# Kernel tuning notes

Measured on AMD Instinct MI355X. Metric: run time of the kernel, lower is better.

The kernel has to match this reference:

```python
import jax, jax.numpy as jnp
import numpy as np

LN_EPS = 1e-5
SLOPE = 0.01  # LeakyReLU default

def _ln(x, g, b):
    m = x.mean(-1, keepdims=True)
    v = ((x - m) ** 2).mean(-1, keepdims=True)
    return (x - m) / jnp.sqrt(v + LN_EPS) * g + b

def _leaky(x):
    return jnp.where(x >= 0, x, SLOPE * x)

def _lstm(x_seq, h0, c0, Wih, Whh, bih, bhh):
    # x_seq: [B,S,E]; PyTorch gate order i,f,g,o. Returns (hT, per-step hiddens [B,S,H]).
    gx = jnp.einsum('bse,ge->bsg', x_seq, Wih) + bih + bhh  # precompute input projections
    def step(carry, gxt):
        h, c = carry
        gates = gxt + h @ Whh.T
        i, f, g, o = jnp.split(gates, 4, axis=-1)
        c = jax.nn.sigmoid(f) * c + jax.nn.sigmoid(i) * jnp.tanh(g)
        h = jax.nn.sigmoid(o) * jnp.tanh(c)
        return (h, c), h
    (hT, _), hs = jax.lax.scan(step, (h0, c0), gx.transpose(1, 0, 2))
    return hT, hs.transpose(1, 0, 2)

def setup_inputs() -> dict:
    B, S, NF, E, H, L, C = 256, 1024, 32, 64, 128, 64, 31
    key = jax.random.key(0)
    ks = iter(jax.random.split(key, 40))
    rn = lambda shape, s=0.08: (jax.random.normal(next(ks), shape, jnp.float32) * s)
    d = {}
    d['x'] = jax.random.normal(next(ks), (B, S, NF), jnp.float32)
    d['eps'] = jax.random.normal(next(ks), (B, L), jnp.float32)
    d['init_W'] = rn((E, NF)); d['init_b'] = rn((E,)); d['init_g'] = jnp.ones((E,)); d['init_beta'] = jnp.zeros((E,))
    d['enc_Wih'] = rn((4 * H, E)); d['enc_Whh'] = rn((4 * H, H)); d['enc_bih'] = rn((4 * H,)); d['enc_bhh'] = rn((4 * H,))
    d['mu_W'] = rn((L, H)); d['mu_b'] = rn((L,)); d['mu_g'] = jnp.ones((L,)); d['mu_beta'] = jnp.zeros((L,))
    d['lv_W'] = rn((L, H)); d['lv_b'] = rn((L,)); d['lv_g'] = jnp.ones((L,)); d['lv_beta'] = jnp.zeros((L,))
    d['dec_Wih'] = rn((4 * H, E)); d['dec_Whh'] = rn((4 * H, H)); d['dec_bih'] = rn((4 * H,)); d['dec_bhh'] = rn((4 * H,))
    d['lh_W'] = rn((H, L)); d['lh_b'] = rn((H,)); d['lh_g'] = jnp.ones((H,)); d['lh_beta'] = jnp.zeros((H,))
    d['lc_W'] = rn((H, L)); d['lc_b'] = rn((H,)); d['lc_g'] = jnp.ones((H,)); d['lc_beta'] = jnp.zeros((H,))
    d['act_W'] = rn((C, H)); d['act_b'] = rn((C,))
    d['time_W'] = rn((1, H)); d['time_b'] = rn((1,))
    return d

def reference(x, eps, init_W, init_b, init_g, init_beta,
              enc_Wih, enc_Whh, enc_bih, enc_bhh,
              mu_W, mu_b, mu_g, mu_beta, lv_W, lv_b, lv_g, lv_beta,
              dec_Wih, dec_Whh, dec_bih, dec_bhh,
              lh_W, lh_b, lh_g, lh_beta, lc_W, lc_b, lc_g, lc_beta,
              act_W, act_b, time_W, time_b):
    B = x.shape[0]
    H = enc_Whh.shape[1]
    # init_layers: Linear -> LeakyReLU -> LayerNorm
    x_emb = _ln(_leaky(x @ init_W.T + init_b), init_g, init_beta)  # [B,S,E]
    # encoder LSTM with h0=ones, c0=zeros (as in encode())
    hT, _ = _lstm(x_emb, jnp.ones((B, H), x.dtype), jnp.zeros((B, H), x.dtype),
                  enc_Wih, enc_Whh, enc_bih, enc_bhh)
    mu = _ln(_leaky(hT @ mu_W.T + mu_b), mu_g, mu_beta)
    logvar = _ln(_leaky(hT @ lv_W.T + lv_b), lv_g, lv_beta)
    latent = mu + eps * jnp.exp(0.5 * logvar)
    # decoder init state from latent
    dh0 = _ln(_leaky(latent @ lh_W.T + lh_b), lh_g, lh_beta)
    dc0 = _ln(_leaky(latent @ lc_W.T + lc_b), lc_g, lc_beta)
    # _decode prefix loop (prefix_len=1..S-1, collecting hn) == one scan over x_emb[:, :S-1]
    _, hs = _lstm(x_emb[:, :-1], dh0, dc0, dec_Wih, dec_Whh, dec_bih, dec_bhh)  # [B,S-1,H]
    acts = hs @ act_W.T + act_b   # [B,S-1,C]
    ts = hs @ time_W.T + time_b   # [B,S-1,1]
    return acts, ts, mu, logvar
```

## Files before the change

### kernel.cpp

```cpp
#include <hip/hip_runtime.h>
#include <hip/hip_bf16.h>
#include <type_traits>


#define B_ 256
#define S_ 1024
#define NF_ 32
#define E_ 64
#define H_ 128
#define L_ 64
#define C_ 31

#define ACTS_OFF 0
#define TS_OFF   8118528
#define MU_OFF   8380416
#define LV_OFF   8396800

#define LOG2E  1.44269504f
#define LOG2E2 2.88539008f

typedef __attribute__((ext_vector_type(8))) short short8;
typedef __attribute__((ext_vector_type(4))) float float4v;

__device__ inline unsigned short f2bf(float x){
  union { float f; unsigned u; } a; a.f = x;
  unsigned r = a.u + 0x7FFFu + ((a.u >> 16) & 1u);
  return (unsigned short)(r >> 16);
}
__device__ inline float frcp(float x){
#if __has_builtin(__builtin_amdgcn_rcpf)
  return __builtin_amdgcn_rcpf(x);
#else
  return 1.0f / x;
#endif
}
__device__ inline float fexp2(float x){
#if __has_builtin(__builtin_amdgcn_exp2f)
  return __builtin_amdgcn_exp2f(x);
#else
  return exp2f(x);
#endif
}
__device__ inline float fsig(float x){ return frcp(1.0f + fexp2(-LOG2E*x)); }
__device__ inline float leaky(float x){ return x >= 0.0f ? x : 0.01f*x; }
__device__ inline float wredsum(float v){
  v += __shfl_xor(v, 32, 64);
  v += __shfl_xor(v, 16, 64);
  v += __shfl_xor(v,  8, 64);
  v += __shfl_xor(v,  4, 64);
  v += __shfl_xor(v,  2, 64);
  v += __shfl_xor(v,  1, 64);
  return v;
}

#define INIT_ROWS 16
__global__ __launch_bounds__(256) void init_kernel(
    const float* __restrict__ x, const float* __restrict__ W,
    const float* __restrict__ bias, const float* __restrict__ gam,
    const float* __restrict__ beta, unsigned short* __restrict__ xemb)
{
  if (blockIdx.x == 0 && threadIdx.x < 64)
    xemb[(size_t)S_*B_*E_ + threadIdx.x] = 0;

  const int wave = threadIdx.x >> 6, lane = threadIdx.x & 63;
  float wf[NF_];
  {
    const float4* wr = (const float4*)(W + lane * NF_);
    #pragma unroll
    for (int j = 0; j < NF_/4; ++j){
      float4 t = wr[j];
      wf[4*j+0] = t.x; wf[4*j+1] = t.y; wf[4*j+2] = t.z; wf[4*j+3] = t.w;
    }
  }
  const float bb = bias[lane], gg = gam[lane], be = beta[lane];

  const int r0 = (blockIdx.x * 4 + wave) * INIT_ROWS;
  for (int rr = 0; rr < INIT_ROWS; ++rr){
    const int ru = __builtin_amdgcn_readfirstlane(r0 + rr);
    const int b = ru >> 10, s = ru & 1023;
    const float* xr = x + (size_t)ru * NF_;
    float acc = bb;
    #pragma unroll
    for (int k = 0; k < NF_; ++k)
      acc = fmaf(xr[k], wf[k], acc);
    acc = leaky(acc);
    float m = wredsum(acc) * (1.0f/64.0f);
    float d = acc - m;
    float v = wredsum(d*d) * (1.0f/64.0f);
    float y = d * rsqrtf(v + 1e-5f) * gg + be;
    xemb[((size_t)s * B_ + b) * E_ + lane] = f2bf(y);
  }
}

__global__ __launch_bounds__(512, 2) void lstm_kernel(
    const float* __restrict__ Wih,
    const float* __restrict__ Whh,
    const float* __restrict__ bih, const float* __restrict__ bhh,
    const unsigned short* __restrict__ xemb,
    int T,
    const float* __restrict__ h0, const float* __restrict__ c0,
    float* __restrict__ hT_out,
    unsigned short* __restrict__ hs_out)
{
  __shared__ unsigned short hbuf[2][16*136];
  const int tid = threadIdx.x;
  const int wave = tid >> 6, lane = tid & 63;
  const int q = lane >> 4, c16 = lane & 15;
  const int bt0 = blockIdx.x * 4;
  const int hu = wave * 16 + c16;

  short8 Bf[4][6];
  float bias[4];
  #pragma unroll
  for (int g = 0; g < 4; ++g){
    const int gcol = g*128 + hu;
    bias[g] = bih[gcol] + bhh[gcol];
    #pragma unroll
    for (int kb = 0; kb < 6; ++kb){
      union { short8 v; unsigned short u[8]; } tmp;
      #pragma unroll
      for (int j = 0; j < 8; ++j){
        int k = kb*32 + q*8 + j;
        float wv = (kb < 4) ? Whh[gcol*H_ + k] : Wih[gcol*E_ + (k - H_)];
        tmp.u[j] = f2bf(wv);
      }
      Bf[g][kb] = tmp.v;
    }
  }

  unsigned short* hflat = &hbuf[0][0];
  for (int idx = tid; idx < 2*16*136; idx += 512) hflat[idx] = 0;
  __syncthreads();
  {
    int b = tid >> 7, k = tid & 127;
    hbuf[0][(4*b)*136 + k] = h0 ? f2bf(h0[((size_t)(bt0 + b))*H_ + k])
                                : (unsigned short)0x3F80;
  }
  float cst = c0 ? c0[((size_t)(bt0 + q))*H_ + hu] : 0.0f;
  __syncthreads();

  const int xb = c16 >> 2, xdt = c16 & 3;
  const unsigned short* xbase = xemb + ((size_t)(bt0 + xb))*E_ + q*8;
  const size_t xrow = (size_t)B_*E_;
  auto xwin = [&](int wt)->const unsigned short*{
    int tt = wt + xdt; if (tt > T-1) tt = T-1;
    return xbase + (size_t)tt * xrow;
  };

  float4v gxA[4], gxB[4];
  short8 nx0, nx1;
  { const unsigned short* p = xwin(0);
    nx0 = *(const short8*)p; nx1 = *(const short8*)(p + 32); }
  #pragma unroll
  for (int g = 0; g < 4; ++g){
    float4v t = (float4v){bias[g], bias[g], bias[g], bias[g]};
    t = __builtin_amdgcn_mfma_f32_16x16x32_bf16(nx0, Bf[g][4], t, 0, 0, 0);
    gxA[g] = __builtin_amdgcn_mfma_f32_16x16x32_bf16(nx1, Bf[g][5], t, 0, 0, 0);
  }
  { const unsigned short* p = xwin(4);
    nx0 = *(const short8*)p; nx1 = *(const short8*)(p + 32); }

  short8 Af0 = 0, Af1 = 0, Af2 = 0, Af3 = 0;

  const unsigned short* haR0 = hflat + (c16 & ~3)*136 + q*8;
  const unsigned short* haR1 = haR0 + 2176;
  unsigned short* hw0 = hflat + (4*q)*136 + hu;
  unsigned short* hw1 = hw0 + 2176;
  unsigned short* hsp = hs_out ? (hs_out + ((size_t)(bt0 + q))*H_ + hu) : nullptr;
  float zero_f = 0.0f;
  const float4v z4 = (float4v){0.0f, 0.0f, 0.0f, 0.0f};

  auto step = [&](int t, auto dtc, float4v (&gxP)[4], auto&& pre, auto&& post){
    constexpr int dt = decltype(dtc)::value;
    const unsigned short* ha = (t & 1) ? haR1 : haR0;
    if ((c16 & 3) == dt){
      Af0 = *(const short8*)(ha);
      Af1 = *(const short8*)(ha + 32);
      Af2 = *(const short8*)(ha + 64);
      Af3 = *(const short8*)(ha + 96);
    }
    pre();

    float4v aA[4], aB[4];
    #pragma unroll
    for (int g = 0; g < 4; ++g)
      aA[g] = __builtin_amdgcn_mfma_f32_16x16x32_bf16(Af0, Bf[g][0], gxP[g], 0, 0, 0);
    #pragma unroll
    for (int g = 0; g < 4; ++g)
      aB[g] = __builtin_amdgcn_mfma_f32_16x16x32_bf16(Af2, Bf[g][2], z4, 0, 0, 0);
    #pragma unroll
    for (int g = 0; g < 4; ++g)
      aA[g] = __builtin_amdgcn_mfma_f32_16x16x32_bf16(Af1, Bf[g][1], aA[g], 0, 0, 0);
    #pragma unroll
    for (int g = 0; g < 4; ++g)
      aB[g] = __builtin_amdgcn_mfma_f32_16x16x32_bf16(Af3, Bf[g][3], aB[g], 0, 0, 0);

    post();

    float gi = aA[0][dt] + aB[0][dt];
    float gf = aA[1][dt] + aB[1][dt];
    float gg = aA[2][dt] + aB[2][dt];
    float go = aA[3][dt] + aB[3][dt];
    float ei  = fexp2(gi * LOG2E);
    float e2g = fexp2(gg * LOG2E2);
    float t1  = (ei * (e2g - 1.0f)) * frcp((1.0f + ei) * (1.0f + e2g));
    float sf  = fsig(gf);
    float c   = fmaf(sf, cst, t1);
    cst = c;
    float eo  = fexp2(go * LOG2E);
    float e2c = fexp2(fminf(c * LOG2E2, 126.0f));
    float h   = (eo * (e2c - 1.0f)) * frcp((1.0f + eo) * (1.0f + e2c));
    unsigned vv;
    asm("v_cvt_pk_bf16_f32 %0, %1, %2" : "=v"(vv) : "v"(h), "v"(zero_f));
    unsigned short hb16 = (unsigned short)vv;
    unsigned short* hw = (t & 1) ? hw0 : hw1;
    hw[0] = hb16;
    if (hs_out){ *hsp = hb16; hsp += (size_t)B_*H_; }
    if (hT_out && t == T-1) hT_out[((size_t)(bt0 + q))*H_ + hu] = h;
    __builtin_amdgcn_sched_barrier(0);
    asm volatile("s_waitcnt lgkmcnt(0)" ::: "memory");
    __builtin_amdgcn_s_barrier();
    __builtin_amdgcn_sched_barrier(0);
  };

  using I0 = std::integral_constant<int,0>;
  using I1 = std::integral_constant<int,1>;
  using I2 = std::integral_constant<int,2>;
  using I3 = std::integral_constant<int,3>;
  auto nop = []{};

  const int nwin = T >> 2, ntail = T & 3;
  for (int w = 0; w < nwin; ++w){
    const int t0 = w << 2;
    step(t0+0, I0{}, gxA, [&]{
      #pragma unroll
      for (int g = 0; g < 4; ++g){
        float4v tt = (float4v){bias[g], bias[g], bias[g], bias[g]};
        tt = __builtin_amdgcn_mfma_f32_16x16x32_bf16(nx0, Bf[g][4], tt, 0, 0, 0);
        gxB[g] = __builtin_amdgcn_mfma_f32_16x16x32_bf16(nx1, Bf[g][5], tt, 0, 0, 0);
      }
    }, nop);
    step(t0+1, I1{}, gxA, [&]{
      const unsigned short* p = xwin(t0 + 8);
      nx0 = *(const short8*)p; nx1 = *(const short8*)(p + 32);
    }, nop);
    step(t0+2, I2{}, gxA, nop, nop);
    step(t0+3, I3{}, gxA, nop, [&]{
      #pragma unroll
      for (int g = 0; g < 4; ++g) gxA[g] = gxB[g];
    });
  }
  if (ntail > 0) step(nwin*4+0, I0{}, gxA, nop, nop);
  if (ntail > 1) step(nwin*4+1, I1{}, gxA, nop, nop);
  if (ntail > 2) step(nwin*4+2, I2{}, gxA, nop, nop);
}

__global__ __launch_bounds__(128) void latent_kernel(
    const float* __restrict__ hT, const float* __restrict__ eps,
    const float* __restrict__ mu_W, const float* __restrict__ mu_b,
    const float* __restrict__ mu_g, const float* __restrict__ mu_be,
    const float* __restrict__ lv_W, const float* __restrict__ lv_b,
    const float* __restrict__ lv_g, const float* __restrict__ lv_be,
    const float* __restrict__ lh_W, const float* __restrict__ lh_b,
    const float* __restrict__ lh_g, const float* __restrict__ lh_be,
    const float* __restrict__ lc_W, const float* __restrict__ lc_b,
    const float* __restrict__ lc_g, const float* __restrict__ lc_be,
    float* __restrict__ out, float* __restrict__ dh0, float* __restrict__ dc0)
{
  const int b = blockIdx.x, tid = threadIdx.x;
  const int wave = tid >> 6, lane = tid & 63;
  __shared__ float shT[H_];
  __shared__ float smu[L_], slv[L_], slat[L_];
  __shared__ float part[2];
  shT[tid] = hT[(size_t)b*H_ + tid];
  __syncthreads();
  {
    const float* W = wave ? lv_W : mu_W;
    float a = (wave ? lv_b : mu_b)[lane];
    for (int k = 0; k < H_; ++k) a += shT[k] * W[lane*H_ + k];
    a = leaky(a);
    float m = wredsum(a) * (1.0f/L_);
    float d = a - m;
    float v = wredsum(d*d) * (1.0f/L_);
    float y = d * rsqrtf(v + 1e-5f) * (wave ? lv_g : mu_g)[lane] + (wave ? lv_be : mu_be)[lane];
    out[(wave ? LV_OFF : MU_OFF) + (size_t)b*L_ + lane] = y;
    if (wave) slv[lane] = y; else smu[lane] = y;
  }
  __syncthreads();
  if (tid < L_) slat[tid] = smu[tid] + eps[(size_t)b*L_ + tid] * expf(0.5f*slv[tid]);
  __syncthreads();
  #pragma unroll 1
  for (int which = 0; which < 2; ++which){
    const float* W = which ? lc_W : lh_W;
    float p = (which ? lc_b : lh_b)[tid];
    for (int k = 0; k < L_; ++k) p += slat[k] * W[tid*L_ + k];
    p = leaky(p);
    float s = wredsum(p);
    if (lane == 0) part[wave] = s;
    __syncthreads();
    float mean = (part[0] + part[1]) * (1.0f/H_);
    __syncthreads();
    float d = p - mean;
    float s2 = wredsum(d*d);
    if (lane == 0) part[wave] = s2;
    __syncthreads();
    float var = (part[0] + part[1]) * (1.0f/H_);
    __syncthreads();
    float y = d * rsqrtf(var + 1e-5f) * (which ? lc_g : lh_g)[tid] + (which ? lc_be : lh_be)[tid];
    (which ? dc0 : dh0)[(size_t)b*H_ + tid] = y;
  }
}

__global__ __launch_bounds__(256) void out_kernel(
    const unsigned short* __restrict__ hs,
    const float* __restrict__ actW, const float* __restrict__ actB,
    const float* __restrict__ timeW, const float* __restrict__ timeB,
    float* __restrict__ out)
{
  const int wave = threadIdx.x >> 6, lane = threadIdx.x & 63;
  const int quad = lane >> 4, c16 = lane & 15;
  const int mt = blockIdx.x * 4 + wave;
  short8 Wf[2][4]; float biasn[2];
  #pragma unroll
  for (int ti = 0; ti < 2; ++ti){
    const int n = ti*16 + c16;
    biasn[ti] = (n < C_) ? actB[n] : timeB[0];
    #pragma unroll
    for (int kb = 0; kb < 4; ++kb){
      union { short8 v; unsigned short u[8]; } tmp;
      #pragma unroll
      for (int j = 0; j < 8; ++j){
        int k = kb*32 + quad*8 + j;
        tmp.u[j] = f2bf((n < C_) ? actW[n*H_ + k] : timeW[k]);
      }
      Wf[ti][kb] = tmp.v;
    }
  }
  const unsigned short* hp = hs + ((size_t)mt*16 + c16)*H_ + quad*8;
  float4v acc[2];
  #pragma unroll
  for (int ti = 0; ti < 2; ++ti) acc[ti] = (float4v){biasn[ti], biasn[ti], biasn[ti], biasn[ti]};
  #pragma unroll
  for (int kb = 0; kb < 4; ++kb){
    short8 a = *(const short8*)(hp + kb*32);
    acc[0] = __builtin_amdgcn_mfma_f32_16x16x32_bf16(a, Wf[0][kb], acc[0], 0, 0, 0);
    acc[1] = __builtin_amdgcn_mfma_f32_16x16x32_bf16(a, Wf[1][kb], acc[1], 0, 0, 0);
  }
  #pragma unroll
  for (int ti = 0; ti < 2; ++ti){
    const int n = ti*16 + c16;
    #pragma unroll
    for (int r = 0; r < 4; ++r){
      int rr = mt*16 + quad*4 + r;
      int tt = rr >> 8, b = rr & 255;
      float v = acc[ti][r];
      if (n < C_) out[ACTS_OFF + ((size_t)b*1023 + tt)*C_ + n] = v;
      else        out[TS_OFF + (size_t)b*1023 + tt] = v;
    }
  }
}

extern "C" void kernel_launch(void* const* d_in, const int* in_sizes, int n_in,
                              void* d_out, int out_size, void* d_ws, size_t ws_size,
                              hipStream_t stream)
{
  (void)in_sizes; (void)n_in; (void)out_size; (void)ws_size;
  const float* x       = (const float*)d_in[0];
  const float* eps     = (const float*)d_in[1];
  const float* init_W  = (const float*)d_in[2];
  const float* init_b  = (const float*)d_in[3];
  const float* init_g  = (const float*)d_in[4];
  const float* init_be = (const float*)d_in[5];
  const float* enc_Wih = (const float*)d_in[6];
  const float* enc_Whh = (const float*)d_in[7];
  const float* enc_bih = (const float*)d_in[8];
  const float* enc_bhh = (const float*)d_in[9];
  const float* mu_W  = (const float*)d_in[10];
  const float* mu_b  = (const float*)d_in[11];
  const float* mu_g  = (const float*)d_in[12];
  const float* mu_be = (const float*)d_in[13];
  const float* lv_W  = (const float*)d_in[14];
  const float* lv_b  = (const float*)d_in[15];
  const float* lv_g  = (const float*)d_in[16];
  const float* lv_be = (const float*)d_in[17];
  const float* dec_Wih = (const float*)d_in[18];
  const float* dec_Whh = (const float*)d_in[19];
  const float* dec_bih = (const float*)d_in[20];
  const float* dec_bhh = (const float*)d_in[21];
  const float* lh_W  = (const float*)d_in[22];
  const float* lh_b  = (const float*)d_in[23];
  const float* lh_g  = (const float*)d_in[24];
  const float* lh_be = (const float*)d_in[25];
  const float* lc_W  = (const float*)d_in[26];
  const float* lc_b  = (const float*)d_in[27];
  const float* lc_g  = (const float*)d_in[28];
  const float* lc_be = (const float*)d_in[29];
  const float* act_W  = (const float*)d_in[30];
  const float* act_b  = (const float*)d_in[31];
  const float* time_W = (const float*)d_in[32];
  const float* time_b = (const float*)d_in[33];
  float* out = (float*)d_out;

  unsigned short* xemb = (unsigned short*)d_ws;
  unsigned short* hs   = xemb + (size_t)S_*B_*E_ + 64;
  float* hT  = (float*)(hs + (size_t)(S_-1)*B_*H_);
  float* dh0 = hT  + B_*H_;
  float* dc0 = dh0 + B_*H_;

  init_kernel<<<dim3((B_*S_)/(4*INIT_ROWS)), dim3(256), 0, stream>>>(
      x, init_W, init_b, init_g, init_be, xemb);

  lstm_kernel<<<dim3(64), dim3(512), 0, stream>>>(
      enc_Wih, enc_Whh, enc_bih, enc_bhh, xemb, S_,
      nullptr, nullptr, hT, nullptr);

  latent_kernel<<<dim3(B_), dim3(128), 0, stream>>>(
      hT, eps, mu_W, mu_b, mu_g, mu_be, lv_W, lv_b, lv_g, lv_be,
      lh_W, lh_b, lh_g, lh_be, lc_W, lc_b, lc_g, lc_be, out, dh0, dc0);

  lstm_kernel<<<dim3(64), dim3(512), 0, stream>>>(
      dec_Wih, dec_Whh, dec_bih, dec_bhh, xemb, S_-1,
      dh0, dc0, nullptr, hs);

  out_kernel<<<dim3((B_*(S_-1))/16/4), dim3(256), 0, stream>>>(
      hs, act_W, act_b, time_W, time_b, out);
}
```

Baseline: 1.174 ms.

## Halve LSTM block to 4 waves, each computing two hidden-unit tiles

```diff
diff --git a/kernel.cpp b/kernel.cpp
--- a/kernel.cpp
+++ b/kernel.cpp
@@ -92,7 +92,7 @@
   }
 }
 
-__global__ __launch_bounds__(512, 2) void lstm_kernel(
+__global__ __launch_bounds__(256, 1) void lstm_kernel(
     const float* __restrict__ Wih,
     const float* __restrict__ Whh,
     const float* __restrict__ bih, const float* __restrict__ bhh,
@@ -107,36 +107,40 @@
   const int wave = tid >> 6, lane = tid & 63;
   const int q = lane >> 4, c16 = lane & 15;
   const int bt0 = blockIdx.x * 4;
-  const int hu = wave * 16 + c16;
-
-  short8 Bf[4][6];
-  float bias[4];
-  #pragma unroll
-  for (int g = 0; g < 4; ++g){
-    const int gcol = g*128 + hu;
-    bias[g] = bih[gcol] + bhh[gcol];
-    #pragma unroll
-    for (int kb = 0; kb < 6; ++kb){
-      union { short8 v; unsigned short u[8]; } tmp;
-      #pragma unroll
-      for (int j = 0; j < 8; ++j){
-        int k = kb*32 + q*8 + j;
-        float wv = (kb < 4) ? Whh[gcol*H_ + k] : Wih[gcol*E_ + (k - H_)];
-        tmp.u[j] = f2bf(wv);
+  const int hu0 = wave * 32 + c16;
+
+  short8 Bf[2][4][6];
+  float bias[2][4];
+  #pragma unroll
+  for (int nt = 0; nt < 2; ++nt){
+    #pragma unroll
+    for (int g = 0; g < 4; ++g){
+      const int gcol = g*128 + hu0 + nt*16;
+      bias[nt][g] = bih[gcol] + bhh[gcol];
+      #pragma unroll
+      for (int kb = 0; kb < 6; ++kb){
+        union { short8 v; unsigned short u[8]; } tmp;
+        #pragma unroll
+        for (int j = 0; j < 8; ++j){
+          int k = kb*32 + q*8 + j;
+          float wv = (kb < 4) ? Whh[gcol*H_ + k] : Wih[gcol*E_ + (k - H_)];
+          tmp.u[j] = f2bf(wv);
+        }
+        Bf[nt][g][kb] = tmp.v;
       }
-      Bf[g][kb] = tmp.v;
     }
   }
 
   unsigned short* hflat = &hbuf[0][0];
-  for (int idx = tid; idx < 2*16*136; idx += 512) hflat[idx] = 0;
+  for (int idx = tid; idx < 2*16*136; idx += 256) hflat[idx] = 0;
   __syncthreads();
-  {
-    int b = tid >> 7, k = tid & 127;
+  for (int e = tid; e < 512; e += 256){
+    int b = e >> 7, k = e & 127;
     hbuf[0][(4*b)*136 + k] = h0 ? f2bf(h0[((size_t)(bt0 + b))*H_ + k])
                                 : (unsigned short)0x3F80;
   }
-  float cst = c0 ? c0[((size_t)(bt0 + q))*H_ + hu] : 0.0f;
+  float cst0 = c0 ? c0[((size_t)(bt0 + q))*H_ + hu0]      : 0.0f;
+  float cst1 = c0 ? c0[((size_t)(bt0 + q))*H_ + hu0 + 16] : 0.0f;
   __syncthreads();
 
   const int xb = c16 >> 2, xdt = c16 & 3;
@@ -147,15 +151,17 @@
     return xbase + (size_t)tt * xrow;
   };
 
-  float4v gxA[4], gxB[4];
+  float4v gxA[2][4], gxB[2][4];
   short8 nx0, nx1;
   { const unsigned short* p = xwin(0);
     nx0 = *(const short8*)p; nx1 = *(const short8*)(p + 32); }
   #pragma unroll
+  for (int nt = 0; nt < 2; ++nt)
+  #pragma unroll
   for (int g = 0; g < 4; ++g){
-    float4v t = (float4v){bias[g], bias[g], bias[g], bias[g]};
-    t = __builtin_amdgcn_mfma_f32_16x16x32_bf16(nx0, Bf[g][4], t, 0, 0, 0);
-    gxA[g] = __builtin_amdgcn_mfma_f32_16x16x32_bf16(nx1, Bf[g][5], t, 0, 0, 0);
+    float4v t = (float4v){bias[nt][g], bias[nt][g], bias[nt][g], bias[nt][g]};
+    t = __builtin_amdgcn_mfma_f32_16x16x32_bf16(nx0, Bf[nt][g][4], t, 0, 0, 0);
+    gxA[nt][g] = __builtin_amdgcn_mfma_f32_16x16x32_bf16(nx1, Bf[nt][g][5], t, 0, 0, 0);
   }
   { const unsigned short* p = xwin(4);
     nx0 = *(const short8*)p; nx1 = *(const short8*)(p + 32); }
@@ -164,13 +170,23 @@
 
   const unsigned short* haR0 = hflat + (c16 & ~3)*136 + q*8;
   const unsigned short* haR1 = haR0 + 2176;
-  unsigned short* hw0 = hflat + (4*q)*136 + hu;
+  unsigned short* hw0 = hflat + (4*q)*136 + hu0;
   unsigned short* hw1 = hw0 + 2176;
-  unsigned short* hsp = hs_out ? (hs_out + ((size_t)(bt0 + q))*H_ + hu) : nullptr;
-  float zero_f = 0.0f;
-  const float4v z4 = (float4v){0.0f, 0.0f, 0.0f, 0.0f};
-
-  auto step = [&](int t, auto dtc, float4v (&gxP)[4], auto&& pre, auto&& post){
+  unsigned short* hsp = hs_out ? (hs_out + ((size_t)(bt0 + q))*H_ + hu0) : nullptr;
+
+  auto cell = [&](float gi, float gf, float gg, float go, float& cs)->float{
+    float ei  = fexp2(gi * LOG2E);
+    float e2g = fexp2(gg * LOG2E2);
+    float t1  = (ei * (e2g - 1.0f)) * frcp((1.0f + ei) * (1.0f + e2g));
+    float sf  = fsig(gf);
+    float c   = fmaf(sf, cs, t1);
+    cs = c;
+    float eo  = fexp2(go * LOG2E);
+    float e2c = fexp2(fminf(c * LOG2E2, 126.0f));
+    return (eo * (e2c - 1.0f)) * frcp((1.0f + eo) * (1.0f + e2c));
+  };
+
+  auto step = [&](int t, auto dtc, auto&& pre, auto&& post){
     constexpr int dt = decltype(dtc)::value;
     const unsigned short* ha = (t & 1) ? haR1 : haR0;
     if ((c16 & 3) == dt){
@@ -181,42 +197,39 @@
     }
     pre();
 
-    float4v aA[4], aB[4];
-    #pragma unroll
-    for (int g = 0; g < 4; ++g)
-      aA[g] = __builtin_amdgcn_mfma_f32_16x16x32_bf16(Af0, Bf[g][0], gxP[g], 0, 0, 0);
-    #pragma unroll
-    for (int g = 0; g < 4; ++g)
-      aB[g] = __builtin_amdgcn_mfma_f32_16x16x32_bf16(Af2, Bf[g][2], z4, 0, 0, 0);
-    #pragma unroll
-    for (int g = 0; g < 4; ++g)
-      aA[g] = __builtin_amdgcn_mfma_f32_16x16x32_bf16(Af1, Bf[g][1], aA[g], 0, 0, 0);
-    #pragma unroll
-    for (int g = 0; g < 4; ++g)
-      aB[g] = __builtin_amdgcn_mfma_f32_16x16x32_bf16(Af3, Bf[g][3], aB[g], 0, 0, 0);
+    float4v a[2][4];
+    #pragma unroll
+    for (int nt = 0; nt < 2; ++nt){
+      #pragma unroll
+      for (int g = 0; g < 4; ++g)
+        a[nt][g] = __builtin_amdgcn_mfma_f32_16x16x32_bf16(Af0, Bf[nt][g][0], gxA[nt][g], 0, 0, 0);
+      #pragma unroll
+      for (int g = 0; g < 4; ++g)
+        a[nt][g] = __builtin_amdgcn_mfma_f32_16x16x32_bf16(Af1, Bf[nt][g][1], a[nt][g], 0, 0, 0);
+      #pragma unroll
+      for (int g = 0; g < 4; ++g)
+        a[nt][g] = __builtin_amdgcn_mfma_f32_16x16x32_bf16(Af2, Bf[nt][g][2], a[nt][g], 0, 0, 0);
+      #pragma unroll
+      for (int g = 0; g < 4; ++g)
+        a[nt][g] = __builtin_amdgcn_mfma_f32_16x16x32_bf16(Af3, Bf[nt][g][3], a[nt][g], 0, 0, 0);
+    }
 
     post();
 
-    float gi = aA[0][dt] + aB[0][dt];
-    float gf = aA[1][dt] + aB[1][dt];
-    float gg = aA[2][dt] + aB[2][dt];
-    float go = aA[3][dt] + aB[3][dt];
-    float ei  = fexp2(gi * LOG2E);
-    float e2g = fexp2(gg * LOG2E2);
-    float t1  = (ei * (e2g - 1.0f)) * frcp((1.0f + ei) * (1.0f + e2g));
-    float sf  = fsig(gf);
-    float c   = fmaf(sf, cst, t1);
-    cst = c;
-    float eo  = fexp2(go * LOG2E);
-    float e2c = fexp2(fminf(c * LOG2E2, 126.0f));
-    float h   = (eo * (e2c - 1.0f)) * frcp((1.0f + eo) * (1.0f + e2c));
+    float h0v = cell(a[0][0][dt], a[0][1][dt], a[0][2][dt], a[0][3][dt], cst0);
+    float h1v = cell(a[1][0][dt], a[1][1][dt], a[1][2][dt], a[1][3][dt], cst1);
     unsigned vv;
-    asm("v_cvt_pk_bf16_f32 %0, %1, %2" : "=v"(vv) : "v"(h), "v"(zero_f));
-    unsigned short hb16 = (unsigned short)vv;
+    asm("v_cvt_pk_bf16_f32 %0, %1, %2" : "=v"(vv) : "v"(h0v), "v"(h1v));
+    unsigned short lo = (unsigned short)(vv & 0xFFFFu);
+    unsigned short hi = (unsigned short)(vv >> 16);
     unsigned short* hw = (t & 1) ? hw0 : hw1;
-    hw[0] = hb16;
-    if (hs_out){ *hsp = hb16; hsp += (size_t)B_*H_; }
-    if (hT_out && t == T-1) hT_out[((size_t)(bt0 + q))*H_ + hu] = h;
+    hw[0]  = lo;
+    hw[16] = hi;
+    if (hs_out){ hsp[0] = lo; hsp[16] = hi; hsp += (size_t)B_*H_; }
+    if (hT_out && t == T-1){
+      hT_out[((size_t)(bt0 + q))*H_ + hu0]      = h0v;
+      hT_out[((size_t)(bt0 + q))*H_ + hu0 + 16] = h1v;
+    }
     __builtin_amdgcn_sched_barrier(0);
     asm volatile("s_waitcnt lgkmcnt(0)" ::: "memory");
     __builtin_amdgcn_s_barrier();
@@ -232,27 +245,31 @@
   const int nwin = T >> 2, ntail = T & 3;
   for (int w = 0; w < nwin; ++w){
     const int t0 = w << 2;
-    step(t0+0, I0{}, gxA, [&]{
+    step(t0+0, I0{}, [&]{
+      #pragma unroll
+      for (int nt = 0; nt < 2; ++nt)
       #pragma unroll
       for (int g = 0; g < 4; ++g){
-        float4v tt = (float4v){bias[g], bias[g], bias[g], bias[g]};
-        tt = __builtin_amdgcn_mfma_f32_16x16x32_bf16(nx0, Bf[g][4], tt, 0, 0, 0);
-        gxB[g] = __builtin_amdgcn_mfma_f32_16x16x32_bf16(nx1, Bf[g][5], tt, 0, 0, 0);
+        float4v tt = (float4v){bias[nt][g], bias[nt][g], bias[nt][g], bias[nt][g]};
+        tt = __builtin_amdgcn_mfma_f32_16x16x32_bf16(nx0, Bf[nt][g][4], tt, 0, 0, 0);
+        gxB[nt][g] = __builtin_amdgcn_mfma_f32_16x16x32_bf16(nx1, Bf[nt][g][5], tt, 0, 0, 0);
       }
     }, nop);
-    step(t0+1, I1{}, gxA, [&]{
+    step(t0+1, I1{}, [&]{
       const unsigned short* p = xwin(t0 + 8);
       nx0 = *(const short8*)p; nx1 = *(const short8*)(p + 32);
     }, nop);
-    step(t0+2, I2{}, gxA, nop, nop);
-    step(t0+3, I3{}, gxA, nop, [&]{
-      #pragma unroll
-      for (int g = 0; g < 4; ++g) gxA[g] = gxB[g];
+    step(t0+2, I2{}, nop, nop);
+    step(t0+3, I3{}, nop, [&]{
+      #pragma unroll
+      for (int nt = 0; nt < 2; ++nt)
+      #pragma unroll
+      for (int g = 0; g < 4; ++g) gxA[nt][g] = gxB[nt][g];
     });
   }
-  if (ntail > 0) step(nwin*4+0, I0{}, gxA, nop, nop);
-  if (ntail > 1) step(nwin*4+1, I1{}, gxA, nop, nop);
-  if (ntail > 2) step(nwin*4+2, I2{}, gxA, nop, nop);
+  if (ntail > 0) step(nwin*4+0, I0{}, nop, nop);
+  if (ntail > 1) step(nwin*4+1, I1{}, nop, nop);
+  if (ntail > 2) step(nwin*4+2, I2{}, nop, nop);
 }
 
 __global__ __launch_bounds__(128) void latent_kernel(
@@ -410,7 +427,7 @@
   init_kernel<<<dim3((B_*S_)/(4*INIT_ROWS)), dim3(256), 0, stream>>>(
       x, init_W, init_b, init_g, init_be, xemb);
 
-  lstm_kernel<<<dim3(64), dim3(512), 0, stream>>>(
+  lstm_kernel<<<dim3(64), dim3(256), 0, stream>>>(
       enc_Wih, enc_Whh, enc_bih, enc_bhh, xemb, S_,
       nullptr, nullptr, hT, nullptr);
 
@@ -418,7 +435,7 @@
       hT, eps, mu_W, mu_b, mu_g, mu_be, lv_W, lv_b, lv_g, lv_be,
       lh_W, lh_b, lh_g, lh_be, lc_W, lc_b, lc_g, lc_be, out, dh0, dc0);
 
-  lstm_kernel<<<dim3(64), dim3(512), 0, stream>>>(
+  lstm_kernel<<<dim3(64), dim3(256), 0, stream>>>(
       dec_Wih, dec_Whh, dec_bih, dec_bhh, xemb, S_-1,
       dh0, dc0, nullptr, hs);
 
```

Result: slower. 1.306 ms (+11.3%).

## Fuse output projection heads into decoder LSTM recurrence, drop hs buffer

Applied to the files above, without the earlier changes.

```diff
diff --git a/kernel.cpp b/kernel.cpp
--- a/kernel.cpp
+++ b/kernel.cpp
@@ -100,7 +100,9 @@
     int T,
     const float* __restrict__ h0, const float* __restrict__ c0,
     float* __restrict__ hT_out,
-    unsigned short* __restrict__ hs_out)
+    float* __restrict__ outp,
+    const float* __restrict__ actW, const float* __restrict__ actB,
+    const float* __restrict__ timeW, const float* __restrict__ timeB)
 {
   __shared__ unsigned short hbuf[2][16*136];
   const int tid = threadIdx.x;
@@ -128,6 +130,23 @@
     }
   }
 
+  const bool do_out = (outp != nullptr) && (wave < 2);
+  short8 Of0 = 0, Of1 = 0, Of2 = 0, Of3 = 0;
+  float obias = 0.0f;
+  if (do_out){
+    const int n = wave*16 + c16;
+    obias = (n < C_) ? actB[n] : timeB[0];
+    union { short8 v; unsigned short u[8]; } tmp[4];
+    #pragma unroll
+    for (int kb = 0; kb < 4; ++kb)
+      #pragma unroll
+      for (int j = 0; j < 8; ++j){
+        int k = kb*32 + q*8 + j;
+        tmp[kb].u[j] = f2bf((n < C_) ? actW[n*H_ + k] : timeW[k]);
+      }
+    Of0 = tmp[0].v; Of1 = tmp[1].v; Of2 = tmp[2].v; Of3 = tmp[3].v;
+  }
+
   unsigned short* hflat = &hbuf[0][0];
   for (int idx = tid; idx < 2*16*136; idx += 512) hflat[idx] = 0;
   __syncthreads();
@@ -161,14 +180,33 @@
     nx0 = *(const short8*)p; nx1 = *(const short8*)(p + 32); }
 
   short8 Af0 = 0, Af1 = 0, Af2 = 0, Af3 = 0;
+  short8 Po0 = 0, Po1 = 0, Po2 = 0, Po3 = 0;
 
   const unsigned short* haR0 = hflat + (c16 & ~3)*136 + q*8;
   const unsigned short* haR1 = haR0 + 2176;
   unsigned short* hw0 = hflat + (4*q)*136 + hu;
   unsigned short* hw1 = hw0 + 2176;
-  unsigned short* hsp = hs_out ? (hs_out + ((size_t)(bt0 + q))*H_ + hu) : nullptr;
   float zero_f = 0.0f;
   const float4v z4 = (float4v){0.0f, 0.0f, 0.0f, 0.0f};
+
+  auto out_head = [&](const unsigned short* ha, int tt_){
+    if ((c16 & 3) == 0){
+      Po0 = *(const short8*)(ha);
+      Po1 = *(const short8*)(ha + 32);
+      Po2 = *(const short8*)(ha + 64);
+      Po3 = *(const short8*)(ha + 96);
+    }
+    float4v o = z4;
+    o = __builtin_amdgcn_mfma_f32_16x16x32_bf16(Po0, Of0, o, 0, 0, 0);
+    o = __builtin_amdgcn_mfma_f32_16x16x32_bf16(Po1, Of1, o, 0, 0, 0);
+    o = __builtin_amdgcn_mfma_f32_16x16x32_bf16(Po2, Of2, o, 0, 0, 0);
+    o = __builtin_amdgcn_mfma_f32_16x16x32_bf16(Po3, Of3, o, 0, 0, 0);
+    const float val = o[0] + obias;
+    const int n = wave*16 + c16;
+    const size_t bq = (size_t)(bt0 + q);
+    if (n < C_) outp[ACTS_OFF + (bq*(S_-1) + (size_t)tt_)*C_ + n] = val;
+    else        outp[TS_OFF + bq*(S_-1) + (size_t)tt_] = val;
+  };
 
   auto step = [&](int t, auto dtc, float4v (&gxP)[4], auto&& pre, auto&& post){
     constexpr int dt = decltype(dtc)::value;
@@ -180,6 +218,7 @@
       Af3 = *(const short8*)(ha + 96);
     }
     pre();
+    if (do_out && t > 0) out_head(ha, t - 1);
 
     float4v aA[4], aB[4];
     #pragma unroll
@@ -215,7 +254,6 @@
     unsigned short hb16 = (unsigned short)vv;
     unsigned short* hw = (t & 1) ? hw0 : hw1;
     hw[0] = hb16;
-    if (hs_out){ *hsp = hb16; hsp += (size_t)B_*H_; }
     if (hT_out && t == T-1) hT_out[((size_t)(bt0 + q))*H_ + hu] = h;
     __builtin_amdgcn_sched_barrier(0);
     asm volatile("s_waitcnt lgkmcnt(0)" ::: "memory");
@@ -253,6 +291,8 @@
   if (ntail > 0) step(nwin*4+0, I0{}, gxA, nop, nop);
   if (ntail > 1) step(nwin*4+1, I1{}, gxA, nop, nop);
   if (ntail > 2) step(nwin*4+2, I2{}, gxA, nop, nop);
+
+  if (do_out) out_head((T & 1) ? haR1 : haR0, T - 1);
 }
 
 __global__ __launch_bounds__(128) void latent_kernel(
@@ -308,55 +348,6 @@
     __syncthreads();
     float y = d * rsqrtf(var + 1e-5f) * (which ? lc_g : lh_g)[tid] + (which ? lc_be : lh_be)[tid];
     (which ? dc0 : dh0)[(size_t)b*H_ + tid] = y;
-  }
-}
-
-__global__ __launch_bounds__(256) void out_kernel(
-    const unsigned short* __restrict__ hs,
-    const float* __restrict__ actW, const float* __restrict__ actB,
-    const float* __restrict__ timeW, const float* __restrict__ timeB,
-    float* __restrict__ out)
-{
-  const int wave = threadIdx.x >> 6, lane = threadIdx.x & 63;
-  const int quad = lane >> 4, c16 = lane & 15;
-  const int mt = blockIdx.x * 4 + wave;
-  short8 Wf[2][4]; float biasn[2];
-  #pragma unroll
-  for (int ti = 0; ti < 2; ++ti){
-    const int n = ti*16 + c16;
-    biasn[ti] = (n < C_) ? actB[n] : timeB[0];
-    #pragma unroll
-    for (int kb = 0; kb < 4; ++kb){
-      union { short8 v; unsigned short u[8]; } tmp;
-      #pragma unroll
-      for (int j = 0; j < 8; ++j){
-        int k = kb*32 + quad*8 + j;
-        tmp.u[j] = f2bf((n < C_) ? actW[n*H_ + k] : timeW[k]);
-      }
-      Wf[ti][kb] = tmp.v;
-    }
-  }
-  const unsigned short* hp = hs + ((size_t)mt*16 + c16)*H_ + quad*8;
-  float4v acc[2];
-  #pragma unroll
-  for (int ti = 0; ti < 2; ++ti) acc[ti] = (float4v){biasn[ti], biasn[ti], biasn[ti], biasn[ti]};
-  #pragma unroll
-  for (int kb = 0; kb < 4; ++kb){
-    short8 a = *(const short8*)(hp + kb*32);
-    acc[0] = __builtin_amdgcn_mfma_f32_16x16x32_bf16(a, Wf[0][kb], acc[0], 0, 0, 0);
-    acc[1] = __builtin_amdgcn_mfma_f32_16x16x32_bf16(a, Wf[1][kb], acc[1], 0, 0, 0);
-  }
-  #pragma unroll
-  for (int ti = 0; ti < 2; ++ti){
-    const int n = ti*16 + c16;
-    #pragma unroll
-    for (int r = 0; r < 4; ++r){
-      int rr = mt*16 + quad*4 + r;
-      int tt = rr >> 8, b = rr & 255;
-      float v = acc[ti][r];
-      if (n < C_) out[ACTS_OFF + ((size_t)b*1023 + tt)*C_ + n] = v;
-      else        out[TS_OFF + (size_t)b*1023 + tt] = v;
-    }
   }
 }
 
@@ -402,8 +393,7 @@
   float* out = (float*)d_out;
 
   unsigned short* xemb = (unsigned short*)d_ws;
-  unsigned short* hs   = xemb + (size_t)S_*B_*E_ + 64;
-  float* hT  = (float*)(hs + (size_t)(S_-1)*B_*H_);
+  float* hT  = (float*)(xemb + (size_t)S_*B_*E_ + 64);
   float* dh0 = hT  + B_*H_;
   float* dc0 = dh0 + B_*H_;
 
@@ -412,7 +402,8 @@
 
   lstm_kernel<<<dim3(64), dim3(512), 0, stream>>>(
       enc_Wih, enc_Whh, enc_bih, enc_bhh, xemb, S_,
-      nullptr, nullptr, hT, nullptr);
+      nullptr, nullptr, hT,
+      nullptr, nullptr, nullptr, nullptr, nullptr);
 
   latent_kernel<<<dim3(B_), dim3(128), 0, stream>>>(
       hT, eps, mu_W, mu_b, mu_g, mu_be, lv_W, lv_b, lv_g, lv_be,
@@ -420,8 +411,6 @@
 
   lstm_kernel<<<dim3(64), dim3(512), 0, stream>>>(
       dec_Wih, dec_Whh, dec_bih, dec_bhh, xemb, S_-1,
-      dh0, dc0, nullptr, hs);
-
-  out_kernel<<<dim3((B_*(S_-1))/16/4), dim3(256), 0, stream>>>(
-      hs, act_W, act_b, time_W, time_b, out);
-}
+      dh0, dc0, nullptr,
+      out, act_W, act_b, time_W, time_b);
+}
```

Result: slower. 1.220 ms (+3.9%).
